# Optimization experiments

Measured on AMD Instinct MI355X. Metric: run time of the kernel, lower is better.

The kernel has to match this reference:

```python
import jax, jax.numpy as jnp
import numpy as np

TWO_PI = 2.0 * np.pi
SMOOTH = 0.12  # smoothing_factor default

N_STATIONS = 100000
N_TIME = 1000
K = 8


def _spatial_smooth(param, idx, w, is_phase=False, s=SMOOTH):
    # param: [N] (or [N,C]); idx: [N,K] int; w: [N,K] row-normalized
    nb = param[idx]  # [N,K] or [N,K,C]
    if param.ndim == 2:
        w = w[..., None]
    if is_phase:
        # circular mean via unit-complex average, expressed with real atan2
        re = (1.0 - s) * jnp.cos(param) + s * jnp.sum(w * jnp.cos(nb), axis=1)
        im = (1.0 - s) * jnp.sin(param) + s * jnp.sum(w * jnp.sin(nb), axis=1)
        return jnp.arctan2(im, re)
    return (1.0 - s) * param + s * jnp.sum(w * nb, axis=1)


def setup_inputs() -> dict:
    key = jax.random.key(0)
    ks = jax.random.split(key, 10)
    time_vector = jnp.arange(N_TIME, dtype=jnp.float32) / 365.25  # years
    constant_offset = jnp.zeros((N_STATIONS,), jnp.float32)
    linear_trend = jax.random.normal(ks[0], (N_STATIONS,), jnp.float32) * 5.0
    seasonal_amplitudes = jnp.ones((N_STATIONS, 3), jnp.float32) * 8.0
    seasonal_phases = jax.random.uniform(ks[1], (N_STATIONS, 3), jnp.float32) * TWO_PI
    residual_amplitudes = jnp.ones((N_STATIONS, 2), jnp.float32) * 1.5
    residual_phases = jax.random.uniform(ks[2], (N_STATIONS, 2), jnp.float32) * TWO_PI
    residual_periods = jnp.array([180.0, 730.0], jnp.float32)
    periods = jnp.array([0.25, 0.5, 1.0], jnp.float32)
    neighbor_indices = jax.random.randint(ks[3], (N_STATIONS, K), 0, N_STATIONS)
    raw_w = jax.random.uniform(ks[4], (N_STATIONS, K), jnp.float32)
    neighbor_weights = raw_w / (jnp.sum(raw_w, axis=1, keepdims=True) + 1e-6)
    return {
        "time_vector": time_vector,
        "constant_offset": constant_offset,
        "linear_trend": linear_trend,
        "seasonal_amplitudes": seasonal_amplitudes,
        "seasonal_phases": seasonal_phases,
        "residual_amplitudes": residual_amplitudes,
        "residual_phases": residual_phases,
        "residual_periods": residual_periods,
        "periods": periods,
        "neighbor_indices": neighbor_indices,
        "neighbor_weights": neighbor_weights,
    }


def reference(time_vector, constant_offset, linear_trend, seasonal_amplitudes,
              seasonal_phases, residual_amplitudes, residual_phases,
              residual_periods, periods, neighbor_indices, neighbor_weights):
    t = time_vector[None, :]  # [1,T] broadcast over stations
    signals = constant_offset[:, None] + linear_trend[:, None] * t  # [N,T]
    # batched spatial smoothing across all 3 seasonal channels at once
    sm_amp = _spatial_smooth(seasonal_amplitudes, neighbor_indices, neighbor_weights)            # [N,3]
    sm_phase = _spatial_smooth(seasonal_phases, neighbor_indices, neighbor_weights, is_phase=True)  # [N,3]
    for i in range(3):  # fixed small set of periods
        freq = 1.0 / periods[i]
        signals = signals + sm_amp[:, i:i+1] * jnp.sin(TWO_PI * freq * t + sm_phase[:, i:i+1])
    for i in range(2):
        freq = 1.0 / residual_periods[i]
        signals = signals + residual_amplitudes[:, i:i+1] * jnp.sin(TWO_PI * freq * t + residual_phases[:, i:i+1])
    return signals
```

## Files before the change

### kernel.cpp

```cpp
#include <hip/hip_runtime.h>

typedef float f32x4 __attribute__((ext_vector_type(4)));

#define NSEAS 3
#define NRES  2
#define NCOMP 5
#define KNB   8
#define TWO_PI_F 6.28318530717958647692f
#define SPB  50
#define BSIG 256

__global__ __launch_bounds__(BSIG) void fused_insar_kernel(
    const float* __restrict__ time_vector,
    const float* __restrict__ constant_offset,
    const float* __restrict__ linear_trend,
    const float* __restrict__ seas_amp,
    const float* __restrict__ seas_phase,
    const float* __restrict__ res_amp,
    const float* __restrict__ res_phase,
    const float* __restrict__ res_periods,
    const float* __restrict__ periods,
    const int*   __restrict__ nb_idx,
    const float* __restrict__ nb_w,
    float* __restrict__ out,
    int N, int T)
{
    __shared__ __align__(16) float sp[SPB * 12];

    const int tid   = threadIdx.x;
    const int stBeg = blockIdx.x * SPB;
    const int nst   = min(SPB, N - stBeg);

    {
        int s = tid / 5;
        if (tid == s * 5 && s < nst) {
            int st = stBeg + s;
            const float S = 0.12f, OMS = 1.0f - 0.12f;

            const int4*  ip = reinterpret_cast<const int4*>(nb_idx + st * KNB);
            const f32x4* wp = reinterpret_cast<const f32x4*>(nb_w + st * KNB);
            int4  i0 = ip[0], i1 = ip[1];
            f32x4 w0 = wp[0], w1 = wp[1];
            int   idx[KNB] = {i0.x, i0.y, i0.z, i0.w, i1.x, i1.y, i1.z, i1.w};
            float w[KNB]   = {w0.x, w0.y, w0.z, w0.w, w1.x, w1.y, w1.z, w1.w};

            float accA[NSEAS]  = {0.f, 0.f, 0.f};
            float accRe[NSEAS] = {0.f, 0.f, 0.f};
            float accIm[NSEAS] = {0.f, 0.f, 0.f};

            #pragma unroll
            for (int k = 0; k < KNB; ++k) {
                int nb = idx[k];
                #pragma unroll
                for (int i = 0; i < NSEAS; ++i) {
                    float a = seas_amp[nb * NSEAS + i];
                    float p = seas_phase[nb * NSEAS + i];
                    float spn, cpn;
                    __sincosf(p, &spn, &cpn);
                    accA[i]  = fmaf(w[k], a,   accA[i]);
                    accRe[i] = fmaf(w[k], cpn, accRe[i]);
                    accIm[i] = fmaf(w[k], spn, accIm[i]);
                }
            }

            float outp[12];
            outp[0] = constant_offset[st];
            outp[1] = linear_trend[st];

            #pragma unroll
            for (int i = 0; i < NSEAS; ++i) {
                float smA = OMS * seas_amp[st * NSEAS + i] + S * accA[i];
                float spn, cpn;
                __sincosf(seas_phase[st * NSEAS + i], &spn, &cpn);
                float re = OMS * cpn + S * accRe[i];
                float im = OMS * spn + S * accIm[i];
                float r   = sqrtf(re * re + im * im);
                float inv = smA / fmaxf(r, 1e-30f);
                outp[2 + 2 * i] = re * inv;
                outp[3 + 2 * i] = im * inv;
            }

            #pragma unroll
            for (int i = 0; i < NRES; ++i) {
                float a = res_amp[st * NRES + i];
                float spn, cpn;
                __sincosf(res_phase[st * NRES + i], &spn, &cpn);
                outp[2 + 2 * (NSEAS + i)] = a * cpn;
                outp[3 + 2 * (NSEAS + i)] = a * spn;
            }

            f32x4* po = reinterpret_cast<f32x4*>(sp + s * 12);
            po[0] = f32x4{outp[0], outp[1], outp[2],  outp[3]};
            po[1] = f32x4{outp[4], outp[5], outp[6],  outp[7]};
            po[2] = f32x4{outp[8], outp[9], outp[10], outp[11]};
        }
    }

    const int t0 = tid * 4;
    const bool active = (t0 + 3) < T;

    float tv[4];
    float sT[NCOMP][4], cT[NCOMP][4];
    if (active) {
        f32x4 t4 = *reinterpret_cast<const f32x4*>(time_vector + t0);
        tv[0] = t4.x; tv[1] = t4.y; tv[2] = t4.z; tv[3] = t4.w;
        #pragma unroll
        for (int c = 0; c < NCOMP; ++c) {
            float f = (c < NSEAS) ? (1.0f / periods[c])
                                  : (1.0f / res_periods[c - NSEAS]);
            float wc = TWO_PI_F * f;
            #pragma unroll
            for (int j = 0; j < 4; ++j) {
                __sincosf(wc * tv[j], &sT[c][j], &cT[c][j]);
            }
        }
    }

    __syncthreads();

    int s = 0;

    for (; s + 4 <= nst; s += 4) {
        float off[4], trend[4], cs[4][NCOMP], cc[4][NCOMP];
        #pragma unroll
        for (int u = 0; u < 4; ++u) {
            const f32x4* pv = reinterpret_cast<const f32x4*>(sp + (s + u) * 12);
            f32x4 P0 = pv[0], P1 = pv[1], P2 = pv[2];
            off[u] = P0.x; trend[u] = P0.y;
            cs[u][0] = P0.z; cc[u][0] = P0.w;
            cs[u][1] = P1.x; cc[u][1] = P1.y;
            cs[u][2] = P1.z; cc[u][2] = P1.w;
            cs[u][3] = P2.x; cc[u][3] = P2.y;
            cs[u][4] = P2.z; cc[u][4] = P2.w;
        }
        if (active) {
            #pragma unroll
            for (int u = 0; u < 4; ++u) {
                float v[4];
                #pragma unroll
                for (int j = 0; j < 4; ++j) {
                    float acc = fmaf(trend[u], tv[j], off[u]);
                    #pragma unroll
                    for (int i = 0; i < NCOMP; ++i) {
                        acc = fmaf(cs[u][i], sT[i][j], acc);
                        acc = fmaf(cc[u][i], cT[i][j], acc);
                    }
                    v[j] = acc;
                }
                f32x4 o = {v[0], v[1], v[2], v[3]};
                *reinterpret_cast<f32x4*>(out + (size_t)(stBeg + s + u) * T + t0) = o;
            }
        }
    }

    for (; s < nst; ++s) {
        const f32x4* pv = reinterpret_cast<const f32x4*>(sp + s * 12);
        f32x4 P0 = pv[0], P1 = pv[1], P2 = pv[2];
        float off = P0.x, trend = P0.y;
        float cs[NCOMP], cc[NCOMP];
        cs[0] = P0.z; cc[0] = P0.w;
        cs[1] = P1.x; cc[1] = P1.y;
        cs[2] = P1.z; cc[2] = P1.w;
        cs[3] = P2.x; cc[3] = P2.y;
        cs[4] = P2.z; cc[4] = P2.w;

        if (active) {
            float v[4];
            #pragma unroll
            for (int j = 0; j < 4; ++j) {
                float acc = fmaf(trend, tv[j], off);
                #pragma unroll
                for (int i = 0; i < NCOMP; ++i) {
                    acc = fmaf(cs[i], sT[i][j], acc);
                    acc = fmaf(cc[i], cT[i][j], acc);
                }
                v[j] = acc;
            }
            f32x4 o = {v[0], v[1], v[2], v[3]};
            *reinterpret_cast<f32x4*>(out + (size_t)(stBeg + s) * T + t0) = o;
        } else if (t0 < T) {
            for (int j = 0; j < 4 && t0 + j < T; ++j) {
                int t = t0 + j;
                float tt = time_vector[t];
                float acc = fmaf(trend, tt, off);
                for (int i = 0; i < NCOMP; ++i) {
                    float f = (i < NSEAS) ? (1.0f / periods[i])
                                          : (1.0f / res_periods[i - NSEAS]);
                    float sv, cv;
                    __sincosf(TWO_PI_F * f * tt, &sv, &cv);
                    acc = fmaf(cs[i], sv, acc);
                    acc = fmaf(cc[i], cv, acc);
                }
                out[(size_t)(stBeg + s) * T + t] = acc;
            }
        }
    }
}

extern "C" void kernel_launch(void* const* d_in, const int* in_sizes, int n_in,
                              void* d_out, int out_size, void* d_ws, size_t ws_size,
                              hipStream_t stream) {
    const float* time_vector     = (const float*)d_in[0];
    const float* constant_offset = (const float*)d_in[1];
    const float* linear_trend    = (const float*)d_in[2];
    const float* seas_amp        = (const float*)d_in[3];
    const float* seas_phase     = (const float*)d_in[4];
    const float* res_amp         = (const float*)d_in[5];
    const float* res_phase       = (const float*)d_in[6];
    const float* res_periods     = (const float*)d_in[7];
    const float* periods         = (const float*)d_in[8];
    const int*   nb_idx          = (const int*)d_in[9];
    const float* nb_w            = (const float*)d_in[10];

    int T = in_sizes[0];
    int N = in_sizes[1];

    float* out = (float*)d_out;

    int grid = (N + SPB - 1) / SPB;
    fused_insar_kernel<<<grid, BSIG, 0, stream>>>(
        time_vector, constant_offset, linear_trend,
        seas_amp, seas_phase, res_amp, res_phase,
        res_periods, periods, nb_idx, nb_w,
        out, N, T);
}
```

Before: 97.28 us.

## Double stations per block, vectorize the inner FMAs and prefetch station params

Each block now handles 100 stations instead of 50. The per-station neighbour-smoothing prologue runs on one thread per station instead of every fifth thread. The inner accumulation uses two-wide vector FMAs, which can map to packed FP32 FMA instructions, and station coefficients are double-buffered from shared memory so the next group loads while the current group computes. The aim is to amortize the time-basis sincos setup over more stations and to cut ALU issue in the store loop. The cost is half as many blocks, which may worsen load balance, and higher register pressure from the double buffers.

```diff
diff --git a/kernel.cpp b/kernel.cpp
--- a/kernel.cpp
+++ b/kernel.cpp
@@ -1,14 +1,19 @@
 #include <hip/hip_runtime.h>
 
 typedef float f32x4 __attribute__((ext_vector_type(4)));
+typedef float f32x2 __attribute__((ext_vector_type(2)));
 
 #define NSEAS 3
 #define NRES  2
 #define NCOMP 5
 #define KNB   8
 #define TWO_PI_F 6.28318530717958647692f
-#define SPB  50
+#define SPB  100
 #define BSIG 256
+
+static __device__ __forceinline__ f32x2 bc2(float x) {
+    f32x2 r; r.x = x; r.y = x; return r;
+}
 
 __global__ __launch_bounds__(BSIG) void fused_insar_kernel(
     const float* __restrict__ time_vector,
@@ -31,148 +36,167 @@
     const int stBeg = blockIdx.x * SPB;
     const int nst   = min(SPB, N - stBeg);
 
-    {
-        int s = tid / 5;
-        if (tid == s * 5 && s < nst) {
-            int st = stBeg + s;
-            const float S = 0.12f, OMS = 1.0f - 0.12f;
-
-            const int4*  ip = reinterpret_cast<const int4*>(nb_idx + st * KNB);
-            const f32x4* wp = reinterpret_cast<const f32x4*>(nb_w + st * KNB);
-            int4  i0 = ip[0], i1 = ip[1];
-            f32x4 w0 = wp[0], w1 = wp[1];
-            int   idx[KNB] = {i0.x, i0.y, i0.z, i0.w, i1.x, i1.y, i1.z, i1.w};
-            float w[KNB]   = {w0.x, w0.y, w0.z, w0.w, w1.x, w1.y, w1.z, w1.w};
-
-            float accA[NSEAS]  = {0.f, 0.f, 0.f};
-            float accRe[NSEAS] = {0.f, 0.f, 0.f};
-            float accIm[NSEAS] = {0.f, 0.f, 0.f};
-
-            #pragma unroll
-            for (int k = 0; k < KNB; ++k) {
-                int nb = idx[k];
-                #pragma unroll
-                for (int i = 0; i < NSEAS; ++i) {
-                    float a = seas_amp[nb * NSEAS + i];
-                    float p = seas_phase[nb * NSEAS + i];
-                    float spn, cpn;
-                    __sincosf(p, &spn, &cpn);
-                    accA[i]  = fmaf(w[k], a,   accA[i]);
-                    accRe[i] = fmaf(w[k], cpn, accRe[i]);
-                    accIm[i] = fmaf(w[k], spn, accIm[i]);
-                }
-            }
-
-            float outp[12];
-            outp[0] = constant_offset[st];
-            outp[1] = linear_trend[st];
-
+    if (tid < nst) {
+        const int st = stBeg + tid;
+        const float S = 0.12f, OMS = 1.0f - 0.12f;
+
+        const int4*  ip = reinterpret_cast<const int4*>(nb_idx + st * KNB);
+        const f32x4* wp = reinterpret_cast<const f32x4*>(nb_w + st * KNB);
+        int4  i0 = ip[0], i1 = ip[1];
+        f32x4 w0 = wp[0], w1 = wp[1];
+        int   idx[KNB] = {i0.x, i0.y, i0.z, i0.w, i1.x, i1.y, i1.z, i1.w};
+        float w[KNB]   = {w0.x, w0.y, w0.z, w0.w, w1.x, w1.y, w1.z, w1.w};
+
+        float accA[NSEAS]  = {0.f, 0.f, 0.f};
+        float accRe[NSEAS] = {0.f, 0.f, 0.f};
+        float accIm[NSEAS] = {0.f, 0.f, 0.f};
+
+        #pragma unroll
+        for (int k = 0; k < KNB; ++k) {
+            int nb = idx[k];
             #pragma unroll
             for (int i = 0; i < NSEAS; ++i) {
-                float smA = OMS * seas_amp[st * NSEAS + i] + S * accA[i];
+                float a = seas_amp[nb * NSEAS + i];
+                float p = seas_phase[nb * NSEAS + i];
                 float spn, cpn;
-                __sincosf(seas_phase[st * NSEAS + i], &spn, &cpn);
-                float re = OMS * cpn + S * accRe[i];
-                float im = OMS * spn + S * accIm[i];
-                float r   = sqrtf(re * re + im * im);
-                float inv = smA / fmaxf(r, 1e-30f);
-                outp[2 + 2 * i] = re * inv;
-                outp[3 + 2 * i] = im * inv;
+                __sincosf(p, &spn, &cpn);
+                accA[i]  = fmaf(w[k], a,   accA[i]);
+                accRe[i] = fmaf(w[k], cpn, accRe[i]);
+                accIm[i] = fmaf(w[k], spn, accIm[i]);
             }
-
-            #pragma unroll
-            for (int i = 0; i < NRES; ++i) {
-                float a = res_amp[st * NRES + i];
-                float spn, cpn;
-                __sincosf(res_phase[st * NRES + i], &spn, &cpn);
-                outp[2 + 2 * (NSEAS + i)] = a * cpn;
-                outp[3 + 2 * (NSEAS + i)] = a * spn;
-            }
-
-            f32x4* po = reinterpret_cast<f32x4*>(sp + s * 12);
-            po[0] = f32x4{outp[0], outp[1], outp[2],  outp[3]};
-            po[1] = f32x4{outp[4], outp[5], outp[6],  outp[7]};
-            po[2] = f32x4{outp[8], outp[9], outp[10], outp[11]};
-        }
+        }
+
+        float outp[12];
+        outp[0] = constant_offset[st];
+        outp[1] = linear_trend[st];
+
+        #pragma unroll
+        for (int i = 0; i < NSEAS; ++i) {
+            float smA = OMS * seas_amp[st * NSEAS + i] + S * accA[i];
+            float spn, cpn;
+            __sincosf(seas_phase[st * NSEAS + i], &spn, &cpn);
+            float re = OMS * cpn + S * accRe[i];
+            float im = OMS * spn + S * accIm[i];
+            float r   = sqrtf(re * re + im * im);
+            float inv = smA / fmaxf(r, 1e-30f);
+            outp[2 + 2 * i] = re * inv;
+            outp[3 + 2 * i] = im * inv;
+        }
+
+        #pragma unroll
+        for (int i = 0; i < NRES; ++i) {
+            float a = res_amp[st * NRES + i];
+            float spn, cpn;
+            __sincosf(res_phase[st * NRES + i], &spn, &cpn);
+            outp[2 + 2 * (NSEAS + i)] = a * cpn;
+            outp[3 + 2 * (NSEAS + i)] = a * spn;
+        }
+
+        f32x4* po = reinterpret_cast<f32x4*>(sp + tid * 12);
+        po[0] = f32x4{outp[0], outp[1], outp[2],  outp[3]};
+        po[1] = f32x4{outp[4], outp[5], outp[6],  outp[7]};
+        po[2] = f32x4{outp[8], outp[9], outp[10], outp[11]};
     }
 
     const int t0 = tid * 4;
     const bool active = (t0 + 3) < T;
 
-    float tv[4];
-    float sT[NCOMP][4], cT[NCOMP][4];
+    f32x2 tv2[2];
+    f32x2 sT2[NCOMP][2], cT2[NCOMP][2];
     if (active) {
         f32x4 t4 = *reinterpret_cast<const f32x4*>(time_vector + t0);
-        tv[0] = t4.x; tv[1] = t4.y; tv[2] = t4.z; tv[3] = t4.w;
+        tv2[0].x = t4.x; tv2[0].y = t4.y;
+        tv2[1].x = t4.z; tv2[1].y = t4.w;
         #pragma unroll
         for (int c = 0; c < NCOMP; ++c) {
             float f = (c < NSEAS) ? (1.0f / periods[c])
                                   : (1.0f / res_periods[c - NSEAS]);
             float wc = TWO_PI_F * f;
-            #pragma unroll
-            for (int j = 0; j < 4; ++j) {
-                __sincosf(wc * tv[j], &sT[c][j], &cT[c][j]);
-            }
+            float s0, c0, s1, c1, s2, c2, s3, c3;
+            __sincosf(wc * t4.x, &s0, &c0);
+            __sincosf(wc * t4.y, &s1, &c1);
+            __sincosf(wc * t4.z, &s2, &c2);
+            __sincosf(wc * t4.w, &s3, &c3);
+            sT2[c][0].x = s0; sT2[c][0].y = s1;
+            sT2[c][1].x = s2; sT2[c][1].y = s3;
+            cT2[c][0].x = c0; cT2[c][0].y = c1;
+            cT2[c][1].x = c2; cT2[c][1].y = c3;
         }
     }
 
     __syncthreads();
 
-    int s = 0;
-
-    for (; s + 4 <= nst; s += 4) {
-        float off[4], trend[4], cs[4][NCOMP], cc[4][NCOMP];
+    const int ngr = nst / 4;
+
+    auto ldg = [&](int g, f32x4* C) {
+        const f32x4* base = reinterpret_cast<const f32x4*>(sp) + g * 12;
+        #pragma unroll
+        for (int i = 0; i < 12; ++i) C[i] = base[i];
+    };
+
+    auto docg = [&](int g, const f32x4* C) {
+        if (!active) return;
         #pragma unroll
         for (int u = 0; u < 4; ++u) {
-            const f32x4* pv = reinterpret_cast<const f32x4*>(sp + (s + u) * 12);
-            f32x4 P0 = pv[0], P1 = pv[1], P2 = pv[2];
-            off[u] = P0.x; trend[u] = P0.y;
-            cs[u][0] = P0.z; cc[u][0] = P0.w;
-            cs[u][1] = P1.x; cc[u][1] = P1.y;
-            cs[u][2] = P1.z; cc[u][2] = P1.w;
-            cs[u][3] = P2.x; cc[u][3] = P2.y;
-            cs[u][4] = P2.z; cc[u][4] = P2.w;
-        }
-        if (active) {
-            #pragma unroll
-            for (int u = 0; u < 4; ++u) {
-                float v[4];
-                #pragma unroll
-                for (int j = 0; j < 4; ++j) {
-                    float acc = fmaf(trend[u], tv[j], off[u]);
-                    #pragma unroll
-                    for (int i = 0; i < NCOMP; ++i) {
-                        acc = fmaf(cs[u][i], sT[i][j], acc);
-                        acc = fmaf(cc[u][i], cT[i][j], acc);
-                    }
-                    v[j] = acc;
-                }
-                f32x4 o = {v[0], v[1], v[2], v[3]};
-                *reinterpret_cast<f32x4*>(out + (size_t)(stBeg + s + u) * T + t0) = o;
-            }
-        }
-    }
-
-    for (; s < nst; ++s) {
+            f32x4 P0 = C[3 * u], P1 = C[3 * u + 1], P2 = C[3 * u + 2];
+            f32x2 of = bc2(P0.x), tr = bc2(P0.y);
+            f32x2 a0 = __builtin_elementwise_fma(tr, tv2[0], of);
+            f32x2 a1 = __builtin_elementwise_fma(tr, tv2[1], of);
+            a0 = __builtin_elementwise_fma(bc2(P0.z), sT2[0][0], a0);
+            a1 = __builtin_elementwise_fma(bc2(P0.z), sT2[0][1], a1);
+            a0 = __builtin_elementwise_fma(bc2(P0.w), cT2[0][0], a0);
+            a1 = __builtin_elementwise_fma(bc2(P0.w), cT2[0][1], a1);
+            a0 = __builtin_elementwise_fma(bc2(P1.x), sT2[1][0], a0);
+            a1 = __builtin_elementwise_fma(bc2(P1.x), sT2[1][1], a1);
+            a0 = __builtin_elementwise_fma(bc2(P1.y), cT2[1][0], a0);
+            a1 = __builtin_elementwise_fma(bc2(P1.y), cT2[1][1], a1);
+            a0 = __builtin_elementwise_fma(bc2(P1.z), sT2[2][0], a0);
+            a1 = __builtin_elementwise_fma(bc2(P1.z), sT2[2][1], a1);
+            a0 = __builtin_elementwise_fma(bc2(P1.w), cT2[2][0], a0);
+            a1 = __builtin_elementwise_fma(bc2(P1.w), cT2[2][1], a1);
+            a0 = __builtin_elementwise_fma(bc2(P2.x), sT2[3][0], a0);
+            a1 = __builtin_elementwise_fma(bc2(P2.x), sT2[3][1], a1);
+            a0 = __builtin_elementwise_fma(bc2(P2.y), cT2[3][0], a0);
+            a1 = __builtin_elementwise_fma(bc2(P2.y), cT2[3][1], a1);
+            a0 = __builtin_elementwise_fma(bc2(P2.z), sT2[4][0], a0);
+            a1 = __builtin_elementwise_fma(bc2(P2.z), sT2[4][1], a1);
+            a0 = __builtin_elementwise_fma(bc2(P2.w), cT2[4][0], a0);
+            a1 = __builtin_elementwise_fma(bc2(P2.w), cT2[4][1], a1);
+            f32x4 o; o.x = a0.x; o.y = a0.y; o.z = a1.x; o.w = a1.y;
+            *reinterpret_cast<f32x4*>(out + (size_t)(stBeg + 4 * g + u) * T + t0) = o;
+        }
+    };
+
+    f32x4 A[12], B[12];
+    if (ngr > 0) ldg(0, A);
+    int g = 0;
+    for (; g + 2 <= ngr; g += 2) {
+        ldg(g + 1, B);
+        docg(g, A);
+        if (g + 2 < ngr) ldg(g + 2, A);
+        docg(g + 1, B);
+    }
+    if (g < ngr) docg(g, A);
+
+    for (int s = ngr * 4; s < nst; ++s) {
         const f32x4* pv = reinterpret_cast<const f32x4*>(sp + s * 12);
         f32x4 P0 = pv[0], P1 = pv[1], P2 = pv[2];
         float off = P0.x, trend = P0.y;
-        float cs[NCOMP], cc[NCOMP];
-        cs[0] = P0.z; cc[0] = P0.w;
-        cs[1] = P1.x; cc[1] = P1.y;
-        cs[2] = P1.z; cc[2] = P1.w;
-        cs[3] = P2.x; cc[3] = P2.y;
-        cs[4] = P2.z; cc[4] = P2.w;
-
+        float cs[NCOMP] = {P0.z, P1.x, P1.z, P2.x, P2.z};
+        float cc[NCOMP] = {P0.w, P1.y, P1.w, P2.y, P2.w};
         if (active) {
+            float tvv[4] = {tv2[0].x, tv2[0].y, tv2[1].x, tv2[1].y};
             float v[4];
             #pragma unroll
             for (int j = 0; j < 4; ++j) {
-                float acc = fmaf(trend, tv[j], off);
+                int p = j >> 1, l = j & 1;
+                float acc = fmaf(trend, tvv[j], off);
                 #pragma unroll
                 for (int i = 0; i < NCOMP; ++i) {
-                    acc = fmaf(cs[i], sT[i][j], acc);
-                    acc = fmaf(cc[i], cT[i][j], acc);
+                    float sv = l ? sT2[i][p].y : sT2[i][p].x;
+                    float cv = l ? cT2[i][p].y : cT2[i][p].x;
+                    acc = fmaf(cs[i], sv, acc);
+                    acc = fmaf(cc[i], cv, acc);
                 }
                 v[j] = acc;
             }
@@ -204,7 +228,7 @@
     const float* constant_offset = (const float*)d_in[1];
     const float* linear_trend    = (const float*)d_in[2];
     const float* seas_amp        = (const float*)d_in[3];
-    const float* seas_phase     = (const float*)d_in[4];
+    const float* seas_phase      = (const float*)d_in[4];
     const float* res_amp         = (const float*)d_in[5];
     const float* res_phase       = (const float*)d_in[6];
     const float* res_periods     = (const float*)d_in[7];
```

Result: no change. 96.03 us (-1.3%).
